# Kernel optimization log

Hardware: AMD Instinct MI355X
Metric: run time of the kernel (lower is better)

The kernel has to match this reference:

```python
import jax, jax.numpy as jnp
import numpy as np

N = 2048
INPUT_DIM = 256
OUTPUT_DIM = 512
NUM_HEADS = 8
HEAD_DIM = OUTPUT_DIM // NUM_HEADS


def _lin_init(key, fan_in, fan_out):
    # torch nn.Linear default init: U(-1/sqrt(fan_in), 1/sqrt(fan_in))
    kw, kb = jax.random.split(key)
    bound = 1.0 / np.sqrt(fan_in)
    W = jax.random.uniform(kw, (fan_in, fan_out), jnp.float32, -bound, bound)
    b = jax.random.uniform(kb, (fan_out,), jnp.float32, -bound, bound)
    return W, b


def setup_inputs() -> dict:
    key = jax.random.key(0)
    ks = jax.random.split(key, 12)
    x = jax.random.normal(ks[0], (N, INPUT_DIM), jnp.float32)
    rel_pos = jax.random.normal(ks[1], (N, 2), jnp.float32)
    rel_vel = jax.random.normal(ks[2], (N, 1), jnp.float32)
    rel_angle = jax.random.normal(ks[3], (N, 1), jnp.float32)
    Wq, bq = _lin_init(ks[4], INPUT_DIM, OUTPUT_DIM)
    Wk, bk = _lin_init(ks[5], INPUT_DIM, OUTPUT_DIM)
    Wv, bv = _lin_init(ks[6], INPUT_DIM, OUTPUT_DIM)
    Wsb1, bsb1 = _lin_init(ks[7], 2, HEAD_DIM)
    Wsb2, bsb2 = _lin_init(ks[8], HEAD_DIM, 1)
    Wmg1, bmg1 = _lin_init(ks[9], 2, HEAD_DIM)
    Wmg2, bmg2 = _lin_init(ks[10], HEAD_DIM, 1)
    Wo, bo = _lin_init(ks[11], OUTPUT_DIM, 1)
    return dict(x=x, rel_pos=rel_pos, rel_vel=rel_vel, rel_angle=rel_angle,
                Wq=Wq, bq=bq, Wk=Wk, bk=bk, Wv=Wv, bv=bv,
                Wsb1=Wsb1, bsb1=bsb1, Wsb2=Wsb2, bsb2=bsb2,
                Wmg1=Wmg1, bmg1=bmg1, Wmg2=Wmg2, bmg2=bmg2,
                Wo=Wo, bo=bo)


def reference(x, rel_pos, rel_vel, rel_angle,
              Wq, bq, Wk, bk, Wv, bv,
              Wsb1, bsb1, Wsb2, bsb2,
              Wmg1, bmg1, Wmg2, bmg2,
              Wo, bo):
    n = x.shape[0]
    Q = (x @ Wq + bq).reshape(n, NUM_HEADS, HEAD_DIM)
    K = (x @ Wk + bk).reshape(n, NUM_HEADS, HEAD_DIM)
    V = (x @ Wv + bv).reshape(n, NUM_HEADS, HEAD_DIM)

    # scores[q, k, h] = <Q[q,h], K[k,h]> / sqrt(head_dim)
    scores = jnp.einsum('qhd,khd->qkh', Q, K) / np.sqrt(HEAD_DIM).astype(np.float32)

    # spatial bias: per-query scalar, broadcast over keys and heads
    sb = (jax.nn.relu(rel_pos @ Wsb1 + bsb1) @ Wsb2 + bsb2)  # (N, 1)
    scores = scores + sb[:, :, None]  # (N,1,1) broadcast -> (N,N,H)

    # softmax over key dim (dim=1)
    attention = jax.nn.softmax(scores, axis=1)

    # motion gate: per-key scalar in (0,1)
    motion_feat = jnp.concatenate([rel_vel, rel_angle], axis=-1)  # (N, 2)
    mg = jax.nn.sigmoid(jax.nn.relu(motion_feat @ Wmg1 + bmg1) @ Wmg2 + bmg2)  # (N, 1)
    attention = attention * mg[None, :, 0, None]  # (1,N,1) broadcast

    # weighted sum over keys without materializing (N,N,H,D)
    out = jnp.einsum('qkh,khd->qhd', attention, V).reshape(n, OUTPUT_DIM)
    out = out @ Wo + bo  # (N, 1)
    return out[:, 0]
```

## Files before the change

kernel.cpp:

```cpp
#include <hip/hip_runtime.h>
#include <hip/hip_bf16.h>

constexpr int N    = 2048;
constexpr int IN   = 256;
constexpr int OUT  = 512;
constexpr int NH   = 8;
constexpr int HD   = 64;
constexpr int NQK  = 1024;
constexpr int NC   = 16;
constexpr int KPB  = N / NC;
constexpr int KT   = KPB / 16;

typedef _Float16  f16x8  __attribute__((ext_vector_type(8)));
typedef _Float16  f16x4  __attribute__((ext_vector_type(4)));
typedef float     f32x4  __attribute__((ext_vector_type(4)));

#if __has_builtin(__builtin_amdgcn_exp2f)
#define EXP2(x) __builtin_amdgcn_exp2f(x)
#else
#define EXP2(x) exp2f(x)
#endif

#define QSCALE (0.125f * 1.44269504088896f)

__global__ __launch_bounds__(256)
void prep_wt_wvo(const float* __restrict__ Wq, const float* __restrict__ Wk,
                 const float* __restrict__ Wv, const float* __restrict__ bv,
                 const float* __restrict__ Wo,
                 _Float16* __restrict__ WT,
                 float* __restrict__ Wvo, float* __restrict__ bvo) {
    __shared__ float smem[32 * 33];
    const int b = blockIdx.x;
    const int tid = threadIdx.x;

    if (b < 256) {
        const int k0 = (b & 7) * 32;
        const int n0 = (b >> 3) * 32;
        const float* W = (n0 < OUT) ? Wq : Wk;
        const int nc = (n0 < OUT) ? n0 : n0 - OUT;
        {
            const int row = tid >> 3;
            const int c4  = (tid & 7) * 4;
            const float4 v = *(const float4*)(W + (size_t)(k0 + row) * OUT + nc + c4);
            smem[row * 33 + c4 + 0] = v.x;
            smem[row * 33 + c4 + 1] = v.y;
            smem[row * 33 + c4 + 2] = v.z;
            smem[row * 33 + c4 + 3] = v.w;
        }
        __syncthreads();
        {
            const int nrow = tid >> 3;
            const int k4   = (tid & 7) * 4;
            f16x4 o;
            #pragma unroll
            for (int j = 0; j < 4; j++)
                o[j] = (_Float16)smem[(k4 + j) * 33 + nrow];
            *(f16x4*)(WT + (size_t)(n0 + nrow) * IN + k0 + k4) = o;
        }
    } else {
        float* wo_s = smem;
        wo_s[tid]       = Wo[tid];
        wo_s[tid + 256] = Wo[tid + 256];
        __syncthreads();
        const int i = (b - 256) * 32 + (tid >> 3);
        const int h = tid & 7;
        const float* wr = Wv + (size_t)i * OUT + h * HD;
        float s = 0.f;
        #pragma unroll
        for (int d = 0; d < HD; d += 4) {
            const float4 v = *(const float4*)(wr + d);
            s += v.x * wo_s[h * HD + d + 0] + v.y * wo_s[h * HD + d + 1]
               + v.z * wo_s[h * HD + d + 2] + v.w * wo_s[h * HD + d + 3];
        }
        Wvo[i * NH + h] = s;
        if (b == 256 && tid < NH) {
            float sb = 0.f;
            #pragma unroll
            for (int d = 0; d < HD; d++)
                sb += bv[tid * HD + d] * wo_s[tid * HD + d];
            bvo[tid] = sb;
        }
    }
}

__global__ __launch_bounds__(256)
void gemm_qk_vpm(const float* __restrict__ x, const _Float16* __restrict__ WT,
                 const float* __restrict__ bq, const float* __restrict__ bk,
                 _Float16* __restrict__ Qh, _Float16* __restrict__ Kh,
                 const float* __restrict__ rel_vel,
                 const float* __restrict__ rel_angle,
                 const float* __restrict__ Wmg1, const float* __restrict__ bmg1,
                 const float* __restrict__ Wmg2, const float* __restrict__ bmg2,
                 const float* __restrict__ Wvo, const float* __restrict__ bvo,
                 float* __restrict__ vpmT) {
    __shared__ _Float16 stage[32 * 132];
    __shared__ float wvo_s[IN * NH];
    const int tid = threadIdx.x;

    if (blockIdx.x >= 512) {
        #pragma unroll
        for (int i = 0; i < 8; i++) wvo_s[tid + 256 * i] = Wvo[tid + 256 * i];
        __syncthreads();

        const int k = (blockIdx.x - 512) * 32 + (tid >> 3);
        const int h = tid & 7;

        const float m0 = rel_vel[k], m1 = rel_angle[k];
        float g = bmg2[0];
        #pragma unroll
        for (int j = 0; j < HD; j++) {
            float t = m0 * Wmg1[j] + m1 * Wmg1[HD + j] + bmg1[j];
            t = fmaxf(t, 0.f);
            g += t * Wmg2[j];
        }
        const float mg = 1.f / (1.f + __expf(-g));

        const float4* xr = (const float4*)(x + (size_t)k * IN);
        float a0 = 0.f, a1 = 0.f, a2 = 0.f, a3 = 0.f;
        #pragma unroll 4
        for (int i = 0; i < IN / 4; i++) {
            const float4 v = xr[i];
            a0 += v.x * wvo_s[(i * 4 + 0) * NH + h];
            a1 += v.y * wvo_s[(i * 4 + 1) * NH + h];
            a2 += v.z * wvo_s[(i * 4 + 2) * NH + h];
            a3 += v.w * wvo_s[(i * 4 + 3) * NH + h];
        }
        vpmT[h * N + k] = mg * (a0 + a1 + a2 + a3 + bvo[h]);
        return;
    }

    const int lane = tid & 63;
    const int wave = tid >> 6;
    const int row16 = lane & 15;
    const int quad  = lane >> 4;
    const int nb0 = (blockIdx.x & 7) * 128;
    const int mb  = (blockIdx.x >> 3) * 32;
    const int nb  = nb0 + wave * 32;

    const size_t ar[2] = {(size_t)(mb + row16) * IN, (size_t)(mb + 16 + row16) * IN};
    const size_t br[2] = {(size_t)(nb + row16) * IN, (size_t)(nb + 16 + row16) * IN};

    f32x4 acc[2][2] = {};
    for (int k0 = 0; k0 < IN; k0 += 32) {
        const int ko = k0 + quad * 8;
        f16x8 a[2], bf[2];
        #pragma unroll
        for (int t = 0; t < 2; t++) {
            const float4 u0 = *(const float4*)(x + ar[t] + ko);
            const float4 u1 = *(const float4*)(x + ar[t] + ko + 4);
            f16x8 av;
            av[0] = (_Float16)u0.x; av[1] = (_Float16)u0.y;
            av[2] = (_Float16)u0.z; av[3] = (_Float16)u0.w;
            av[4] = (_Float16)u1.x; av[5] = (_Float16)u1.y;
            av[6] = (_Float16)u1.z; av[7] = (_Float16)u1.w;
            a[t]  = av;
            bf[t] = *(const f16x8*)(WT + br[t] + ko);
        }
        #pragma unroll
        for (int mt = 0; mt < 2; mt++)
            #pragma unroll
            for (int nt = 0; nt < 2; nt++)
                acc[mt][nt] = __builtin_amdgcn_mfma_f32_16x16x32_f16(a[mt], bf[nt], acc[mt][nt], 0, 0, 0);
    }

    const bool isQ = (nb0 < OUT);
    const float scale = isQ ? QSCALE : 1.0f;
    #pragma unroll
    for (int mt = 0; mt < 2; mt++)
        #pragma unroll
        for (int nt = 0; nt < 2; nt++) {
            const int nl = wave * 32 + nt * 16 + row16;
            const int np = nb0 + nl;
            const int nq = isQ ? np : np - OUT;
            const float bias = isQ ? bq[nq] : bk[nq];
            #pragma unroll
            for (int r = 0; r < 4; r++) {
                const int ml = mt * 16 + quad * 4 + r;
                stage[ml * 132 + nl] = (_Float16)((acc[mt][nt][r] + bias) * scale);
            }
        }
    __syncthreads();

    _Float16* dst = isQ ? Qh : Kh;
    const int r2   = tid >> 2;
    const int cidx = tid & 3;
    const int hl   = r2 >> 5;
    const int m    = r2 & 31;
    const int nqh  = (isQ ? nb0 : nb0 - OUT) + hl * 64;
    const int h    = nqh >> 6;
    const size_t goff = ((size_t)h * N + mb + m) * HD + cidx * 16;
    const int soff = m * 132 + hl * 64 + cidx * 16;
    *(f16x8*)(dst + goff)     = *(const f16x8*)(&stage[soff]);
    *(f16x8*)(dst + goff + 8) = *(const f16x8*)(&stage[soff + 8]);
}

__global__ __launch_bounds__(256)
void attn_mfma(const _Float16* __restrict__ Qh, const _Float16* __restrict__ Kh,
               const float* __restrict__ vpmT,
               float* __restrict__ pnum, float* __restrict__ pden) {
    const int b = blockIdx.x;
    const int h = b & 7;
    const int r = b >> 3;
    const int c = r >> 3;
    const int qg = r & 7;
    const int lane = threadIdx.x & 63;
    const int wave = threadIdx.x >> 6;
    const int q0 = (qg * 4 + wave) * 64;
    const int row16 = lane & 15;
    const int quad  = lane >> 4;

    f16x8 Bq[4][2];
    #pragma unroll
    for (int qt = 0; qt < 4; qt++) {
        const size_t qoff = ((size_t)h * N + q0 + qt * 16 + row16) * HD + quad * 8;
        Bq[qt][0] = *(const f16x8*)(Qh + qoff);
        Bq[qt][1] = *(const f16x8*)(Qh + qoff + 32);
    }

    float num[4] = {}, den[4] = {};
    const int k0 = c * KPB;
    const size_t kbase = ((size_t)h * N + k0 + row16) * HD + quad * 8;
    const float* vp = vpmT + h * N + k0 + quad * 4;

    f16x8 A0 = *(const f16x8*)(Kh + kbase);
    f16x8 A1 = *(const f16x8*)(Kh + kbase + 32);
    f32x4 vv = *(const f32x4*)(vp);

    #pragma unroll
    for (int t = 0; t < KT; t++) {
        const int tn = (t + 1 < KT) ? t + 1 : t;
        const size_t ka = kbase + (size_t)tn * 16 * HD;
        const f16x8 nA0 = *(const f16x8*)(Kh + ka);
        const f16x8 nA1 = *(const f16x8*)(Kh + ka + 32);
        const f32x4 nvv = *(const f32x4*)(vp + tn * 16);

        #pragma unroll
        for (int qt = 0; qt < 4; qt++) {
            f32x4 s = {0.f, 0.f, 0.f, 0.f};
            s = __builtin_amdgcn_mfma_f32_16x16x32_f16(A0, Bq[qt][0], s, 0, 0, 0);
            s = __builtin_amdgcn_mfma_f32_16x16x32_f16(A1, Bq[qt][1], s, 0, 0, 0);
            #pragma unroll
            for (int r4 = 0; r4 < 4; r4++) {
                const float e = EXP2(s[r4]);
                num[qt] += e * vv[r4];
                den[qt] += e;
            }
        }
        A0 = nA0; A1 = nA1; vv = nvv;
    }

    #pragma unroll
    for (int qt = 0; qt < 4; qt++) {
        float n = num[qt], d = den[qt];
        n += __shfl_xor(n, 16, 64);  d += __shfl_xor(d, 16, 64);
        n += __shfl_xor(n, 32, 64);  d += __shfl_xor(d, 32, 64);
        if (quad == 0) {
            const int q = q0 + qt * 16 + row16;
            pnum[((size_t)c * NH + h) * N + q] = n;
            pden[((size_t)c * NH + h) * N + q] = d;
        }
    }
}

__global__ __launch_bounds__(64)
void finalize(const float* __restrict__ pnum, const float* __restrict__ pden,
              const float* __restrict__ bo, float* __restrict__ out) {
    const int q = blockIdx.x * 64 + threadIdx.x;
    float acc = bo[0];
    #pragma unroll
    for (int h = 0; h < NH; h++) {
        float num = 0.f, den = 0.f;
        #pragma unroll
        for (int ci = 0; ci < NC; ci++) {
            num += pnum[((size_t)ci * NH + h) * N + q];
            den += pden[((size_t)ci * NH + h) * N + q];
        }
        acc += num / den;
    }
    out[q] = acc;
}

extern "C" void kernel_launch(void* const* d_in, const int* in_sizes, int n_in,
                              void* d_out, int out_size, void* d_ws, size_t ws_size,
                              hipStream_t stream) {
    const float* x         = (const float*)d_in[0];
    const float* rel_vel   = (const float*)d_in[2];
    const float* rel_angle = (const float*)d_in[3];
    const float* Wq        = (const float*)d_in[4];
    const float* bq        = (const float*)d_in[5];
    const float* Wk        = (const float*)d_in[6];
    const float* bk        = (const float*)d_in[7];
    const float* Wv        = (const float*)d_in[8];
    const float* bv        = (const float*)d_in[9];
    const float* Wmg1      = (const float*)d_in[14];
    const float* bmg1      = (const float*)d_in[15];
    const float* Wmg2      = (const float*)d_in[16];
    const float* bmg2      = (const float*)d_in[17];
    const float* Wo        = (const float*)d_in[18];
    const float* bo        = (const float*)d_in[19];
    float* out = (float*)d_out;

    _Float16* WT  = (_Float16*)d_ws;
    _Float16* Qh  = WT + (size_t)NQK * IN;
    _Float16* Kh  = Qh + (size_t)NH * N * HD;
    float* fp     = (float*)(Kh + (size_t)NH * N * HD);
    float* Wvo    = fp;
    float* bvo    = Wvo + IN * NH;
    float* vpmT   = bvo + NH;
    float* pnum   = vpmT + NH * N;
    float* pden   = pnum + (size_t)NC * NH * N;

    hipLaunchKernelGGL(prep_wt_wvo, dim3(264), dim3(256), 0, stream,
                       Wq, Wk, Wv, bv, Wo, WT, Wvo, bvo);
    hipLaunchKernelGGL(gemm_qk_vpm, dim3(576), dim3(256), 0, stream,
                       x, WT, bq, bk, Qh, Kh,
                       rel_vel, rel_angle, Wmg1, bmg1, Wmg2, bmg2, Wvo, bvo, vpmT);
    hipLaunchKernelGGL(attn_mfma, dim3(1024), dim3(256), 0, stream,
                       Qh, Kh, vpmT, pnum, pden);
    hipLaunchKernelGGL(finalize, dim3(N / 64), dim3(64), 0, stream, pnum, pden, bo, out);
}
```

Measured before the change: 138.6 us.

## Fuse finalize into attention via atomic accumulation and last-block reduction

Replaces the per-chunk partial buffers and the separate finalize kernel with float atomicAdds into per-head numerator and denominator arrays. A per-query-group counter lets the last block to finish compute the output for its 256 queries. Zeroing of the accumulators and counters moves into the prep kernel as extra blocks. This removes one kernel launch and the partial-buffer round trip, at the cost of atomic contention and nondeterministic float summation order.

New measurement: 197.9 us. 1.43x slower.

```diff
diff --git a/kernel.cpp b/kernel.cpp
--- a/kernel.cpp
+++ b/kernel.cpp
@@ -10,6 +10,7 @@
 constexpr int NC   = 16;
 constexpr int KPB  = N / NC;
 constexpr int KT   = KPB / 16;
+constexpr int BLKS_PER_QG = NH * NC;
 
 typedef _Float16  f16x8  __attribute__((ext_vector_type(8)));
 typedef _Float16  f16x4  __attribute__((ext_vector_type(4)));
@@ -28,7 +29,8 @@
                  const float* __restrict__ Wv, const float* __restrict__ bv,
                  const float* __restrict__ Wo,
                  _Float16* __restrict__ WT,
-                 float* __restrict__ Wvo, float* __restrict__ bvo) {
+                 float* __restrict__ Wvo, float* __restrict__ bvo,
+                 float* __restrict__ pnum, int* __restrict__ cnt) {
     __shared__ float smem[32 * 33];
     const int b = blockIdx.x;
     const int tid = threadIdx.x;
@@ -57,7 +59,7 @@
                 o[j] = (_Float16)smem[(k4 + j) * 33 + nrow];
             *(f16x4*)(WT + (size_t)(n0 + nrow) * IN + k0 + k4) = o;
         }
-    } else {
+    } else if (b < 264) {
         float* wo_s = smem;
         wo_s[tid]       = Wo[tid];
         wo_s[tid + 256] = Wo[tid + 256];
@@ -80,6 +82,12 @@
                 sb += bv[tid * HD + d] * wo_s[tid * HD + d];
             bvo[tid] = sb;
         }
+    } else {
+        float4* dst = (float4*)pnum + (size_t)(b - 264) * 1024 + tid;
+        const float4 z = {0.f, 0.f, 0.f, 0.f};
+        #pragma unroll
+        for (int i = 0; i < 4; i++) dst[i * 256] = z;
+        if (b == 264 && tid < NH) cnt[tid] = 0;
     }
 }
 
@@ -195,9 +203,12 @@
 }
 
 __global__ __launch_bounds__(256)
-void attn_mfma(const _Float16* __restrict__ Qh, const _Float16* __restrict__ Kh,
-               const float* __restrict__ vpmT,
-               float* __restrict__ pnum, float* __restrict__ pden) {
+void attn_final(const _Float16* __restrict__ Qh, const _Float16* __restrict__ Kh,
+                const float* __restrict__ vpmT,
+                float* __restrict__ pnum, float* __restrict__ pden,
+                int* __restrict__ cnt, const float* __restrict__ bo,
+                float* __restrict__ out) {
+    __shared__ int last_flag;
     const int b = blockIdx.x;
     const int h = b & 7;
     const int r = b >> 3;
@@ -256,28 +267,31 @@
         n += __shfl_xor(n, 32, 64);  d += __shfl_xor(d, 32, 64);
         if (quad == 0) {
             const int q = q0 + qt * 16 + row16;
-            pnum[((size_t)c * NH + h) * N + q] = n;
-            pden[((size_t)c * NH + h) * N + q] = d;
-        }
-    }
-}
-
-__global__ __launch_bounds__(64)
-void finalize(const float* __restrict__ pnum, const float* __restrict__ pden,
-              const float* __restrict__ bo, float* __restrict__ out) {
-    const int q = blockIdx.x * 64 + threadIdx.x;
-    float acc = bo[0];
-    #pragma unroll
-    for (int h = 0; h < NH; h++) {
-        float num = 0.f, den = 0.f;
-        #pragma unroll
-        for (int ci = 0; ci < NC; ci++) {
-            num += pnum[((size_t)ci * NH + h) * N + q];
-            den += pden[((size_t)ci * NH + h) * N + q];
-        }
-        acc += num / den;
-    }
-    out[q] = acc;
+            atomicAdd(&pnum[(size_t)h * N + q], n);
+            atomicAdd(&pden[(size_t)h * N + q], d);
+        }
+    }
+
+    __threadfence();
+    if (threadIdx.x == 0) {
+        const int old = __hip_atomic_fetch_add(&cnt[qg], 1, __ATOMIC_ACQ_REL,
+                                               __HIP_MEMORY_SCOPE_AGENT);
+        last_flag = (old == BLKS_PER_QG - 1);
+    }
+    __syncthreads();
+    if (last_flag) {
+        const int q = qg * 256 + threadIdx.x;
+        float acc = bo[0];
+        #pragma unroll
+        for (int hh = 0; hh < NH; hh++) {
+            const float n = __hip_atomic_load(&pnum[(size_t)hh * N + q],
+                                              __ATOMIC_RELAXED, __HIP_MEMORY_SCOPE_AGENT);
+            const float d = __hip_atomic_load(&pden[(size_t)hh * N + q],
+                                              __ATOMIC_RELAXED, __HIP_MEMORY_SCOPE_AGENT);
+            acc += n / d;
+        }
+        out[q] = acc;
+    }
 }
 
 extern "C" void kernel_launch(void* const* d_in, const int* in_sizes, int n_in,
@@ -308,14 +322,14 @@
     float* bvo    = Wvo + IN * NH;
     float* vpmT   = bvo + NH;
     float* pnum   = vpmT + NH * N;
-    float* pden   = pnum + (size_t)NC * NH * N;
-
-    hipLaunchKernelGGL(prep_wt_wvo, dim3(264), dim3(256), 0, stream,
-                       Wq, Wk, Wv, bv, Wo, WT, Wvo, bvo);
+    float* pden   = pnum + (size_t)NH * N;
+    int*   cnt    = (int*)(pden + (size_t)NH * N);
+
+    hipLaunchKernelGGL(prep_wt_wvo, dim3(272), dim3(256), 0, stream,
+                       Wq, Wk, Wv, bv, Wo, WT, Wvo, bvo, pnum, cnt);
     hipLaunchKernelGGL(gemm_qk_vpm, dim3(576), dim3(256), 0, stream,
                        x, WT, bq, bk, Qh, Kh,
                        rel_vel, rel_angle, Wmg1, bmg1, Wmg2, bmg2, Wvo, bvo, vpmT);
-    hipLaunchKernelGGL(attn_mfma, dim3(1024), dim3(256), 0, stream,
-                       Qh, Kh, vpmT, pnum, pden);
-    hipLaunchKernelGGL(finalize, dim3(N / 64), dim3(64), 0, stream, pnum, pden, bo, out);
+    hipLaunchKernelGGL(attn_final, dim3(1024), dim3(256), 0, stream,
+                       Qh, Kh, vpmT, pnum, pden, cnt, bo, out);
 }
```
